# Performance work log

Hardware: AMD Instinct MI355X
Metric: run time of the kernel (lower is better)

Reference implementation:

```python
import jax, jax.numpy as jnp
import numpy as np
import math

B, S, E, H = 2, 2048, 1024, 16
Dh = E // H

def setup_inputs() -> dict:
    key = jax.random.key(0)
    ks = jax.random.split(key, 11)
    s_in = 1.0 / math.sqrt(E)
    return {
        "key": jax.random.normal(ks[0], (B, S, E), jnp.float32),
        "query": jax.random.normal(ks[1], (B, S, E), jnp.float32),
        "value": jax.random.normal(ks[2], (B, S, E), jnp.float32),
        "Wq": jax.random.normal(ks[3], (E, E), jnp.float32) * s_in,
        "bq": jnp.zeros((E,), jnp.float32),
        "Wk": jax.random.normal(ks[4], (E, E), jnp.float32) * s_in,
        "bk": jnp.zeros((E,), jnp.float32),
        "Wv": jax.random.normal(ks[5], (E, E), jnp.float32) * s_in,
        "bv": jnp.zeros((E,), jnp.float32),
        "Wo": jax.random.normal(ks[6], (E, E), jnp.float32) * s_in,
        "bo": jnp.zeros((E,), jnp.float32),
    }

def _split_heads(x):
    # [B,S,E] -> [B,H,S,Dh]
    b, s, _ = x.shape
    return x.reshape(b, s, H, Dh).transpose(0, 2, 1, 3)

def reference(key, query, value, Wq, bq, Wk, bk, Wv, bv, Wo, bo):
    k = _split_heads(key @ Wk.T + bk)
    q = _split_heads(query @ Wq.T + bq)
    v = _split_heads(value @ Wv.T + bv)
    scale = 1.0 / math.sqrt(Dh)
    # [B,H,S,S] score matrix (faithful to naive implementation)
    scores = jnp.einsum("bhqd,bhkd->bhqk", q, k) * scale
    probs = jax.nn.softmax(scores, axis=-1)
    attn = jnp.einsum("bhqk,bhkd->bhqd", probs, v)  # [B,H,S,Dh]
    out = attn.transpose(0, 2, 1, 3).reshape(key.shape[0], key.shape[1], E)
    return out @ Wo.T + bo
```

## Files before the change

### kernel.cpp

```cpp
#include <hip/hip_runtime.h>
#include <hip/hip_bf16.h>
#include <stdint.h>

typedef short    bf16x8 __attribute__((ext_vector_type(8)));
typedef float    f32x4  __attribute__((ext_vector_type(4)));
typedef float    f32x16 __attribute__((ext_vector_type(16)));
typedef uint32_t u32x2  __attribute__((ext_vector_type(2)));
typedef uint32_t u32x4  __attribute__((ext_vector_type(4)));
typedef uint16_t u16x4  __attribute__((ext_vector_type(4)));

#define DEV __device__ __forceinline__
#define AS1 __attribute__((address_space(1)))
#define AS3 __attribute__((address_space(3)))

#define SM_SCALE 0.18033688011112042f

DEV uint32_t pk_bf16(float lo, float hi) {
    uint32_t r;
    asm("v_cvt_pk_bf16_f32 %0, %1, %2" : "=v"(r) : "v"(lo), "v"(hi));
    return r;
}

DEV void gload_lds16(const uint16_t* g, uint16_t* l) {
    __builtin_amdgcn_global_load_lds((AS1 const uint32_t*)g, (AS3 uint32_t*)l, 16, 0, 0);
}

DEV void plane32_swap(uint32_t& a, uint32_t& b) {
    asm("v_permlane32_swap_b32 %0, %1" : "+v"(a), "+v"(b));
}

__global__ __launch_bounds__(256) void cast_all(
    const float* __restrict__ w0, const float* __restrict__ w1,
    const float* __restrict__ w2, const float* __restrict__ w3,
    const float* __restrict__ aq, const float* __restrict__ ak, const float* __restrict__ av,
    uint16_t* __restrict__ ws)
{
    const int y = blockIdx.y;
    const float* s;
    uint16_t* d;
    if (y < 4) {
        if (blockIdx.x >= 512) return;
        s = (y == 0) ? w0 : (y == 1) ? w1 : (y == 2) ? w2 : w3;
        d = ws + ((size_t)y << 20);
    } else {
        s = (y == 4) ? aq : (y == 5) ? ak : av;
        d = ws + (size_t)(1 << 22) + ((size_t)(y - 4) << 22);
    }
    const float m = (y == 0) ? SM_SCALE : 1.0f;
    const size_t i = ((size_t)blockIdx.x * 256 + threadIdx.x) * 8;
    float4 a = *reinterpret_cast<const float4*>(s + i);
    float4 b = *reinterpret_cast<const float4*>(s + i + 4);
    u32x4 w;
    w[0] = pk_bf16(a.x * m, a.y * m); w[1] = pk_bf16(a.z * m, a.w * m);
    w[2] = pk_bf16(b.x * m, b.y * m); w[3] = pk_bf16(b.z * m, b.w * m);
    *reinterpret_cast<u32x4*>(d + i) = w;
}

__global__ __launch_bounds__(256) void gemm_qkv(
    const uint16_t* __restrict__ Qc, const uint16_t* __restrict__ Kc, const uint16_t* __restrict__ Vc,
    const uint16_t* __restrict__ wqc, const uint16_t* __restrict__ wkc, const uint16_t* __restrict__ wvc,
    const float* __restrict__ bq, const float* __restrict__ bk, const float* __restrict__ bv,
    uint16_t* __restrict__ Qb, uint16_t* __restrict__ Kb, uint16_t* __restrict__ Vt)
{
    constexpr int Kd = 1024, N = 1024;
    __shared__ uint16_t Al[2][128 * 32];
    __shared__ uint16_t Bl[2][128 * 32];

    const int z = blockIdx.z;
    const uint16_t* A = (z == 0) ? Qc : (z == 1) ? Kc : Vc;
    const uint16_t* W = (z == 0) ? wqc : (z == 1) ? wkc : wvc;
    const float* bias = (z == 0) ? bq : (z == 1) ? bk : bv;
    const float bs = (z == 0) ? SM_SCALE : 1.0f;

    const int brow = blockIdx.x * 128;
    const int bcol = blockIdx.y * 128;
    const int t = threadIdx.x, lane = t & 63, wid = t >> 6;
    const int wr = wid >> 1, wc = wid & 1;

    const int srow = wid * 16 + (lane >> 2);
    const int scol = (lane & 3) * 8;
    const uint16_t* aA = A + (size_t)(brow + srow) * Kd + scol;
    const uint16_t* aW = W + (size_t)(bcol + srow) * Kd + scol;
    uint16_t* lA = &Al[0][srow * 32 + scol];
    uint16_t* lB = &Bl[0][srow * 32 + scol];

    f32x4 acc[4][4];
#pragma unroll
    for (int i = 0; i < 4; ++i)
#pragma unroll
        for (int j = 0; j < 4; ++j)
#pragma unroll
            for (int e = 0; e < 4; ++e) acc[i][j][e] = 0.f;

    const int frow = lane & 15;
    const int koff = (lane >> 4) * 8;

    for (int k0 = 0; k0 < Kd; k0 += 64) {
#pragma unroll
        for (int p = 0; p < 2; ++p) {
            gload_lds16(aA + k0 + p * 32, lA + p * 4096);
            gload_lds16(aA + k0 + p * 32 + (size_t)64 * Kd, lA + p * 4096 + 2048);
            gload_lds16(aW + k0 + p * 32, lB + p * 4096);
            gload_lds16(aW + k0 + p * 32 + (size_t)64 * Kd, lB + p * 4096 + 2048);
        }
        __syncthreads();

#pragma unroll
        for (int p = 0; p < 2; ++p) {
            bf16x8 af[4], bfr[4];
#pragma unroll
            for (int fr = 0; fr < 4; ++fr)
                af[fr] = *reinterpret_cast<const bf16x8*>(&Al[p][(wr * 64 + fr * 16 + frow) * 32 + koff]);
#pragma unroll
            for (int fc = 0; fc < 4; ++fc)
                bfr[fc] = *reinterpret_cast<const bf16x8*>(&Bl[p][(wc * 64 + fc * 16 + frow) * 32 + koff]);
#pragma unroll
            for (int fr = 0; fr < 4; ++fr)
#pragma unroll
                for (int fc = 0; fc < 4; ++fc)
                    acc[fr][fc] = __builtin_amdgcn_mfma_f32_16x16x32_bf16(af[fr], bfr[fc], acc[fr][fc], 0, 0, 0);
        }
        __syncthreads();
    }

    const int m0 = brow + wr * 64;
    const int n0 = bcol + wc * 64;
    if (z < 2) {
        uint16_t* Cb = (z == 0) ? Qb : Kb;
#pragma unroll
        for (int fc = 0; fc < 4; ++fc) {
            const int col = n0 + fc * 16 + frow;
            const float bia = bias[col] * bs;
#pragma unroll
            for (int fr = 0; fr < 4; ++fr) {
                const int mrow = m0 + fr * 16 + (lane >> 4) * 4;
                f32x4 a = acc[fr][fc];
                uint32_t w01 = pk_bf16(a[0] + bia, a[1] + bia);
                uint32_t w23 = pk_bf16(a[2] + bia, a[3] + bia);
                Cb[(size_t)(mrow + 0) * N + col] = (uint16_t)(w01 & 0xffff);
                Cb[(size_t)(mrow + 1) * N + col] = (uint16_t)(w01 >> 16);
                Cb[(size_t)(mrow + 2) * N + col] = (uint16_t)(w23 & 0xffff);
                Cb[(size_t)(mrow + 3) * N + col] = (uint16_t)(w23 >> 16);
            }
        }
    } else {
#pragma unroll
        for (int fc = 0; fc < 4; ++fc) {
            const int col = n0 + fc * 16 + frow;
            const int hh = col >> 6, dd = col & 63;
            const float bia = bias[col];
#pragma unroll
            for (int fr = 0; fr < 4; ++fr) {
                const int mrow = m0 + fr * 16 + (lane >> 4) * 4;
                const int bb = mrow >> 11, ss = mrow & 2047;
                f32x4 a = acc[fr][fc];
                uint32_t w01 = pk_bf16(a[0] + bia, a[1] + bia);
                uint32_t w23 = pk_bf16(a[2] + bia, a[3] + bia);
                u16x4 pv;
                pv[0] = (uint16_t)(w01 & 0xffff); pv[1] = (uint16_t)(w01 >> 16);
                pv[2] = (uint16_t)(w23 & 0xffff); pv[3] = (uint16_t)(w23 >> 16);
                *reinterpret_cast<u16x4*>(&Vt[(size_t)((bb * 16 + hh) * 64 + dd) * 2048 + ss]) = pv;
            }
        }
    }
}

__global__ __launch_bounds__(256, 4) void attn_kernel(
    const uint16_t* __restrict__ Qb, const uint16_t* __restrict__ Kb,
    const uint16_t* __restrict__ Vt, uint16_t* __restrict__ At)
{
    constexpr int S = 2048, E = 1024;
    __shared__ uint16_t Kl[2][64 * 72];
    __shared__ uint16_t Vl[2][64 * 72];

    const int bh = blockIdx.y;
    const int b = bh >> 4, h = bh & 15;
    const int t = threadIdx.x;
    const int lane = t & 63, wid = t >> 6;
    const int lo = lane & 31, hi = lane >> 5;
    const int half = wid >> 1;
    const int q0 = blockIdx.x * 64 + (wid & 1) * 32;

    bf16x8 qf[4];
    {
        const uint16_t* qrow = Qb + (size_t)(b * S + q0 + lo) * E + h * 64;
#pragma unroll
        for (int kk = 0; kk < 4; ++kk)
            qf[kk] = *reinterpret_cast<const bf16x8*>(qrow + kk * 16 + hi * 8);
    }

    f32x16 oacc[2];
#pragma unroll
    for (int i = 0; i < 16; ++i) { oacc[0][i] = 0.f; oacc[1][i] = 0.f; }
    float mrun = -1e30f, lsum = 0.f;

    const uint16_t* Kbase = Kb + (size_t)(b * S) * E + h * 64;
    const uint16_t* Vbase = Vt + (size_t)(bh * 64) * S;

    const int r = t >> 2, seg = t & 3;
    const int lds_off = r * 72 + seg * 16;

#pragma unroll 1
    for (int i = 0; i < 16; ++i) {
        {
            const uint16_t* ksa = Kbase + (size_t)(i * 64 + r) * E + seg * 16;
            const uint16_t* vsa = Vbase + (size_t)r * S + i * 64 + seg * 16;
            const uint16_t* ksb = ksa + (size_t)1024 * E;
            const uint16_t* vsb = vsa + 1024;
            u32x4 k0a = *reinterpret_cast<const u32x4*>(ksa);
            u32x4 k1a = *reinterpret_cast<const u32x4*>(ksa + 8);
            u32x4 v0a = *reinterpret_cast<const u32x4*>(vsa);
            u32x4 v1a = *reinterpret_cast<const u32x4*>(vsa + 8);
            u32x4 k0b = *reinterpret_cast<const u32x4*>(ksb);
            u32x4 k1b = *reinterpret_cast<const u32x4*>(ksb + 8);
            u32x4 v0b = *reinterpret_cast<const u32x4*>(vsb);
            u32x4 v1b = *reinterpret_cast<const u32x4*>(vsb + 8);
            *reinterpret_cast<u32x4*>(&Kl[0][lds_off])     = k0a;
            *reinterpret_cast<u32x4*>(&Kl[0][lds_off + 8]) = k1a;
            *reinterpret_cast<u32x4*>(&Vl[0][lds_off])     = v0a;
            *reinterpret_cast<u32x4*>(&Vl[0][lds_off + 8]) = v1a;
            *reinterpret_cast<u32x4*>(&Kl[1][lds_off])     = k0b;
            *reinterpret_cast<u32x4*>(&Kl[1][lds_off + 8]) = k1b;
            *reinterpret_cast<u32x4*>(&Vl[1][lds_off])     = v0b;
            *reinterpret_cast<u32x4*>(&Vl[1][lds_off + 8]) = v1b;
        }
        __syncthreads();

        f32x16 sacc[2];
#pragma unroll
        for (int j = 0; j < 16; ++j) { sacc[0][j] = 0.f; sacc[1][j] = 0.f; }
        __builtin_amdgcn_s_setprio(1);
#pragma unroll
        for (int kk = 0; kk < 4; ++kk) {
            bf16x8 ka0 = *reinterpret_cast<const bf16x8*>(&Kl[half][lo * 72 + kk * 16 + hi * 8]);
            bf16x8 ka1 = *reinterpret_cast<const bf16x8*>(&Kl[half][(32 + lo) * 72 + kk * 16 + hi * 8]);
            sacc[0] = __builtin_amdgcn_mfma_f32_32x32x16_bf16(ka0, qf[kk], sacc[0], 0, 0, 0);
            sacc[1] = __builtin_amdgcn_mfma_f32_32x32x16_bf16(ka1, qf[kk], sacc[1], 0, 0, 0);
        }
        __builtin_amdgcn_s_setprio(0);

        float tm[16];
#pragma unroll
        for (int j = 0; j < 16; ++j) tm[j] = fmaxf(sacc[0][j], sacc[1][j]);
#pragma unroll
        for (int s = 8; s > 0; s >>= 1)
#pragma unroll
            for (int j = 0; j < 8; ++j)
                if (j < s) tm[j] = fmaxf(tm[j], tm[j + s]);
        float pmax = tm[0];
        pmax = fmaxf(pmax, __shfl_xor(pmax, 32, 64));

        if (!__all(pmax - mrun <= 3.0f)) {
            float mnew = fmaxf(mrun, pmax);
            float corr = __builtin_amdgcn_exp2f(mrun - mnew);
            lsum *= corr;
#pragma unroll
            for (int j = 0; j < 16; ++j) { oacc[0][j] *= corr; oacc[1][j] *= corr; }
            mrun = mnew;
        }

        uint32_t w[16];
        float ps0 = 0.f, ps1 = 0.f, ps2 = 0.f, ps3 = 0.f;
#pragma unroll
        for (int kf = 0; kf < 2; ++kf)
#pragma unroll
            for (int j = 0; j < 8; ++j) {
                float pa = __builtin_amdgcn_exp2f(sacc[kf][2 * j]     - mrun);
                float pb = __builtin_amdgcn_exp2f(sacc[kf][2 * j + 1] - mrun);
                if (j & 1) { ps0 += pa; ps1 += pb; } else { ps2 += pa; ps3 += pb; }
                w[kf * 8 + j] = pk_bf16(pa, pb);
            }
        lsum += (ps0 + ps1) + (ps2 + ps3);

        __builtin_amdgcn_s_setprio(1);
#pragma unroll
        for (int ks = 0; ks < 4; ++ks) {
            const int base = (ks >> 1) * 8 + (ks & 1) * 4;
            uint32_t p0 = w[base + 0], p2 = w[base + 2];
            uint32_t p1 = w[base + 1], p3 = w[base + 3];
            plane32_swap(p0, p2);
            plane32_swap(p1, p3);
            u32x4 pw; pw[0] = p0; pw[1] = p1; pw[2] = p2; pw[3] = p3;
            bf16x8 pf = __builtin_bit_cast(bf16x8, pw);
#pragma unroll
            for (int df = 0; df < 2; ++df) {
                bf16x8 vf = *reinterpret_cast<const bf16x8*>(&Vl[half][(df * 32 + lo) * 72 + ks * 16 + hi * 8]);
                oacc[df] = __builtin_amdgcn_mfma_f32_32x32x16_bf16(vf, pf, oacc[df], 0, 0, 0);
            }
        }
        __builtin_amdgcn_s_setprio(0);
        __syncthreads();
    }

    lsum += __shfl_xor(lsum, 32, 64);

    float* ob  = reinterpret_cast<float*>(&Kl[0][0]);
    float* mlb = reinterpret_cast<float*>(&Vl[0][0]);
    const int w2 = wid & 1;
    if (half == 1) {
        float* dst = ob + (w2 * 64 + lane) * 36;
#pragma unroll
        for (int df = 0; df < 2; ++df)
#pragma unroll
            for (int j = 0; j < 16; ++j) dst[df * 16 + j] = oacc[df][j];
        mlb[(w2 * 64 + lane) * 2]     = mrun;
        mlb[(w2 * 64 + lane) * 2 + 1] = lsum;
    }
    __syncthreads();
    if (half == 0) {
        const float* src = ob + (w2 * 64 + lane) * 36;
        const float m1 = mlb[(w2 * 64 + lane) * 2];
        const float l1 = mlb[(w2 * 64 + lane) * 2 + 1];
        const float m  = fmaxf(mrun, m1);
        const float c0 = __builtin_amdgcn_exp2f(mrun - m);
        const float c1 = __builtin_amdgcn_exp2f(m1 - m);
        const float inv = 1.0f / (c0 * lsum + c1 * l1);
        uint16_t* orow = At + (size_t)(b * S + q0 + lo) * E + h * 64;
#pragma unroll
        for (int df = 0; df < 2; ++df)
#pragma unroll
            for (int g = 0; g < 4; ++g) {
                float e0 = (c0 * oacc[df][4 * g + 0] + c1 * src[df * 16 + 4 * g + 0]) * inv;
                float e1 = (c0 * oacc[df][4 * g + 1] + c1 * src[df * 16 + 4 * g + 1]) * inv;
                float e2 = (c0 * oacc[df][4 * g + 2] + c1 * src[df * 16 + 4 * g + 2]) * inv;
                float e3 = (c0 * oacc[df][4 * g + 3] + c1 * src[df * 16 + 4 * g + 3]) * inv;
                uint32_t w01 = pk_bf16(e0, e1);
                uint32_t w23 = pk_bf16(e2, e3);
                u32x2 o2; o2[0] = w01; o2[1] = w23;
                *reinterpret_cast<u32x2*>(orow + df * 32 + 8 * g + 4 * hi) = o2;
            }
    }
}

__global__ __launch_bounds__(256) void gemm_out(
    const uint16_t* __restrict__ Atn, const uint16_t* __restrict__ woc,
    const float* __restrict__ bo, float* __restrict__ out)
{
    constexpr int Kd = 1024, N = 1024;
    __shared__ uint16_t Al[2][128 * 32];
    __shared__ uint16_t Bl[2][128 * 32];

    const int brow = blockIdx.x * 128;
    const int bcol = blockIdx.y * 128;
    const int t = threadIdx.x, lane = t & 63, wid = t >> 6;
    const int wr = wid >> 1, wc = wid & 1;

    const int srow = wid * 16 + (lane >> 2);
    const int scol = (lane & 3) * 8;
    const uint16_t* aA = Atn + (size_t)(brow + srow) * Kd + scol;
    const uint16_t* aW = woc + (size_t)(bcol + srow) * Kd + scol;
    uint16_t* lA = &Al[0][srow * 32 + scol];
    uint16_t* lB = &Bl[0][srow * 32 + scol];

    f32x4 acc[4][4];
#pragma unroll
    for (int i = 0; i < 4; ++i)
#pragma unroll
        for (int j = 0; j < 4; ++j)
#pragma unroll
            for (int e = 0; e < 4; ++e) acc[i][j][e] = 0.f;

    const int frow = lane & 15;
    const int koff = (lane >> 4) * 8;

    for (int k0 = 0; k0 < Kd; k0 += 64) {
#pragma unroll
        for (int p = 0; p < 2; ++p) {
            gload_lds16(aA + k0 + p * 32, lA + p * 4096);
            gload_lds16(aA + k0 + p * 32 + (size_t)64 * Kd, lA + p * 4096 + 2048);
            gload_lds16(aW + k0 + p * 32, lB + p * 4096);
            gload_lds16(aW + k0 + p * 32 + (size_t)64 * Kd, lB + p * 4096 + 2048);
        }
        __syncthreads();

#pragma unroll
        for (int p = 0; p < 2; ++p) {
            bf16x8 af[4], bfr[4];
#pragma unroll
            for (int fr = 0; fr < 4; ++fr)
                af[fr] = *reinterpret_cast<const bf16x8*>(&Al[p][(wr * 64 + fr * 16 + frow) * 32 + koff]);
#pragma unroll
            for (int fc = 0; fc < 4; ++fc)
                bfr[fc] = *reinterpret_cast<const bf16x8*>(&Bl[p][(wc * 64 + fc * 16 + frow) * 32 + koff]);
#pragma unroll
            for (int fr = 0; fr < 4; ++fr)
#pragma unroll
                for (int fc = 0; fc < 4; ++fc)
                    acc[fr][fc] = __builtin_amdgcn_mfma_f32_16x16x32_bf16(af[fr], bfr[fc], acc[fr][fc], 0, 0, 0);
        }
        __syncthreads();
    }

    const int m0 = brow + wr * 64;
    const int n0 = bcol + wc * 64;
#pragma unroll
    for (int fc = 0; fc < 4; ++fc) {
        const int col = n0 + fc * 16 + frow;
        const float bia = bo[col];
#pragma unroll
        for (int fr = 0; fr < 4; ++fr) {
            const int mrow = m0 + fr * 16 + (lane >> 4) * 4;
#pragma unroll
            for (int j = 0; j < 4; ++j)
                out[(size_t)(mrow + j) * N + col] = acc[fr][fc][j] + bia;
        }
    }
}

extern "C" void kernel_launch(void* const* d_in, const int* in_sizes, int n_in,
                              void* d_out, int out_size, void* d_ws, size_t ws_size,
                              hipStream_t stream)
{
    const float* key   = (const float*)d_in[0];
    const float* query = (const float*)d_in[1];
    const float* value = (const float*)d_in[2];
    const float* Wq = (const float*)d_in[3];
    const float* bq = (const float*)d_in[4];
    const float* Wk = (const float*)d_in[5];
    const float* bk = (const float*)d_in[6];
    const float* Wv = (const float*)d_in[7];
    const float* bv = (const float*)d_in[8];
    const float* Wo = (const float*)d_in[9];
    const float* bo = (const float*)d_in[10];

    uint16_t* ws = (uint16_t*)d_ws;
    uint16_t* wqc = ws;
    uint16_t* wkc = ws + ((size_t)1 << 20);
    uint16_t* wvc = ws + ((size_t)2 << 20);
    uint16_t* woc = ws + ((size_t)3 << 20);
    uint16_t* Qc  = ws + ((size_t)1 << 22);
    uint16_t* Kc  = ws + ((size_t)2 << 22);
    uint16_t* Vc  = ws + ((size_t)3 << 22);
    uint16_t* Qb  = ws + ((size_t)4 << 22);
    uint16_t* Kb  = ws + ((size_t)5 << 22);
    uint16_t* Vt  = ws + ((size_t)6 << 22);
    uint16_t* At  = Qc;
    float* out = (float*)d_out;

    cast_all<<<dim3(2048, 7), 256, 0, stream>>>(Wq, Wk, Wv, Wo, query, key, value, ws);
    gemm_qkv<<<dim3(32, 8, 3), 256, 0, stream>>>(Qc, Kc, Vc, wqc, wkc, wvc,
                                                 bq, bk, bv, Qb, Kb, Vt);
    attn_kernel<<<dim3(32, 32), 256, 0, stream>>>(Qb, Kb, Vt, At);
    gemm_out<<<dim3(32, 8), 256, 0, stream>>>(At, woc, bo, out);
}
```

Before: 135.0 us.

## Load K/V MFMA fragments directly from global memory and swizzle attention block order

The attention kernel drops its LDS staging of K and V tiles and the per-iteration __syncthreads barriers. Each wave now reads its MFMA operand fragments straight from global memory, relying on L2 and MALL for reuse across the blocks of the same head. The grid is flattened to 1D with a swizzle that spreads consecutive blocks across 8 groups, likely so blocks sharing a head land on the same XCD's L2. In exchange, each wave issues more global loads whose latency is no longer hidden by staging, and reuse within a block is lost.

```diff
diff --git a/kernel.cpp b/kernel.cpp
--- a/kernel.cpp
+++ b/kernel.cpp
@@ -170,16 +170,18 @@
     const uint16_t* __restrict__ Vt, uint16_t* __restrict__ At)
 {
     constexpr int S = 2048, E = 1024;
-    __shared__ uint16_t Kl[2][64 * 72];
-    __shared__ uint16_t Vl[2][64 * 72];
-
-    const int bh = blockIdx.y;
+    __shared__ float ob[128 * 36];
+    __shared__ float mlb[128 * 2];
+
+    const int bid = blockIdx.x;
+    const int swz = (bid & 7) * 128 + (bid >> 3);
+    const int bh = swz >> 5;
     const int b = bh >> 4, h = bh & 15;
     const int t = threadIdx.x;
     const int lane = t & 63, wid = t >> 6;
     const int lo = lane & 31, hi = lane >> 5;
     const int half = wid >> 1;
-    const int q0 = blockIdx.x * 64 + (wid & 1) * 32;
+    const int q0 = (swz & 31) * 64 + (wid & 1) * 32;
 
     bf16x8 qf[4];
     {
@@ -194,37 +196,15 @@
     for (int i = 0; i < 16; ++i) { oacc[0][i] = 0.f; oacc[1][i] = 0.f; }
     float mrun = -1e30f, lsum = 0.f;
 
-    const uint16_t* Kbase = Kb + (size_t)(b * S) * E + h * 64;
-    const uint16_t* Vbase = Vt + (size_t)(bh * 64) * S;
-
-    const int r = t >> 2, seg = t & 3;
-    const int lds_off = r * 72 + seg * 16;
+    const uint16_t* k0p = Kb + (size_t)(b * S + half * 1024 + lo) * E + h * 64 + hi * 8;
+    const uint16_t* k1p = k0p + (size_t)32 * E;
+    const uint16_t* v0p = Vt + (size_t)(bh * 64 + lo) * S + half * 1024 + hi * 8;
+    const uint16_t* v1p = v0p + (size_t)32 * S;
 
 #pragma unroll 1
     for (int i = 0; i < 16; ++i) {
-        {
-            const uint16_t* ksa = Kbase + (size_t)(i * 64 + r) * E + seg * 16;
-            const uint16_t* vsa = Vbase + (size_t)r * S + i * 64 + seg * 16;
-            const uint16_t* ksb = ksa + (size_t)1024 * E;
-            const uint16_t* vsb = vsa + 1024;
-            u32x4 k0a = *reinterpret_cast<const u32x4*>(ksa);
-            u32x4 k1a = *reinterpret_cast<const u32x4*>(ksa + 8);
-            u32x4 v0a = *reinterpret_cast<const u32x4*>(vsa);
-            u32x4 v1a = *reinterpret_cast<const u32x4*>(vsa + 8);
-            u32x4 k0b = *reinterpret_cast<const u32x4*>(ksb);
-            u32x4 k1b = *reinterpret_cast<const u32x4*>(ksb + 8);
-            u32x4 v0b = *reinterpret_cast<const u32x4*>(vsb);
-            u32x4 v1b = *reinterpret_cast<const u32x4*>(vsb + 8);
-            *reinterpret_cast<u32x4*>(&Kl[0][lds_off])     = k0a;
-            *reinterpret_cast<u32x4*>(&Kl[0][lds_off + 8]) = k1a;
-            *reinterpret_cast<u32x4*>(&Vl[0][lds_off])     = v0a;
-            *reinterpret_cast<u32x4*>(&Vl[0][lds_off + 8]) = v1a;
-            *reinterpret_cast<u32x4*>(&Kl[1][lds_off])     = k0b;
-            *reinterpret_cast<u32x4*>(&Kl[1][lds_off + 8]) = k1b;
-            *reinterpret_cast<u32x4*>(&Vl[1][lds_off])     = v0b;
-            *reinterpret_cast<u32x4*>(&Vl[1][lds_off + 8]) = v1b;
-        }
-        __syncthreads();
+        const size_t ko = (size_t)i * 64 * E;
+        const int    vo = i * 64;
 
         f32x16 sacc[2];
 #pragma unroll
@@ -232,8 +212,8 @@
         __builtin_amdgcn_s_setprio(1);
 #pragma unroll
         for (int kk = 0; kk < 4; ++kk) {
-            bf16x8 ka0 = *reinterpret_cast<const bf16x8*>(&Kl[half][lo * 72 + kk * 16 + hi * 8]);
-            bf16x8 ka1 = *reinterpret_cast<const bf16x8*>(&Kl[half][(32 + lo) * 72 + kk * 16 + hi * 8]);
+            bf16x8 ka0 = *reinterpret_cast<const bf16x8*>(k0p + ko + kk * 16);
+            bf16x8 ka1 = *reinterpret_cast<const bf16x8*>(k1p + ko + kk * 16);
             sacc[0] = __builtin_amdgcn_mfma_f32_32x32x16_bf16(ka0, qf[kk], sacc[0], 0, 0, 0);
             sacc[1] = __builtin_amdgcn_mfma_f32_32x32x16_bf16(ka1, qf[kk], sacc[1], 0, 0, 0);
         }
@@ -282,20 +262,16 @@
             plane32_swap(p1, p3);
             u32x4 pw; pw[0] = p0; pw[1] = p1; pw[2] = p2; pw[3] = p3;
             bf16x8 pf = __builtin_bit_cast(bf16x8, pw);
-#pragma unroll
-            for (int df = 0; df < 2; ++df) {
-                bf16x8 vf = *reinterpret_cast<const bf16x8*>(&Vl[half][(df * 32 + lo) * 72 + ks * 16 + hi * 8]);
-                oacc[df] = __builtin_amdgcn_mfma_f32_32x32x16_bf16(vf, pf, oacc[df], 0, 0, 0);
-            }
+            bf16x8 vf0 = *reinterpret_cast<const bf16x8*>(v0p + vo + ks * 16);
+            bf16x8 vf1 = *reinterpret_cast<const bf16x8*>(v1p + vo + ks * 16);
+            oacc[0] = __builtin_amdgcn_mfma_f32_32x32x16_bf16(vf0, pf, oacc[0], 0, 0, 0);
+            oacc[1] = __builtin_amdgcn_mfma_f32_32x32x16_bf16(vf1, pf, oacc[1], 0, 0, 0);
         }
         __builtin_amdgcn_s_setprio(0);
-        __syncthreads();
     }
 
     lsum += __shfl_xor(lsum, 32, 64);
 
-    float* ob  = reinterpret_cast<float*>(&Kl[0][0]);
-    float* mlb = reinterpret_cast<float*>(&Vl[0][0]);
     const int w2 = wid & 1;
     if (half == 1) {
         float* dst = ob + (w2 * 64 + lane) * 36;
@@ -440,6 +416,6 @@
     cast_all<<<dim3(2048, 7), 256, 0, stream>>>(Wq, Wk, Wv, Wo, query, key, value, ws);
     gemm_qkv<<<dim3(32, 8, 3), 256, 0, stream>>>(Qc, Kc, Vc, wqc, wkc, wvc,
                                                  bq, bk, bv, Qb, Kb, Vt);
-    attn_kernel<<<dim3(32, 32), 256, 0, stream>>>(Qb, Kb, Vt, At);
+    attn_kernel<<<dim3(1024), 256, 0, stream>>>(Qb, Kb, Vt, At);
     gemm_out<<<dim3(32, 8), 256, 0, stream>>>(At, woc, bo, out);
 }
```

New measurement: 201.7 us. 1.49x slower.

## Fuse fp32-to-bf16 activation cast into QKV projection GEMM

Applied to the files above, without the earlier changes.

Removes the separate cast pass over query/key/value. The QKV GEMM now loads fp32 activations directly into LDS and converts them to bf16 while building MFMA fragments. This avoids writing and re-reading bf16 copies of the activations, at the cost of doubled A-tile global/LDS bytes and extra conversion work inside the GEMM inner loop. The workspace layout is compacted accordingly.

```diff
diff --git a/kernel.cpp b/kernel.cpp
--- a/kernel.cpp
+++ b/kernel.cpp
@@ -21,7 +21,7 @@
     return r;
 }
 
-DEV void gload_lds16(const uint16_t* g, uint16_t* l) {
+DEV void gload_lds16(const void* g, void* l) {
     __builtin_amdgcn_global_load_lds((AS1 const uint32_t*)g, (AS3 uint32_t*)l, 16, 0, 0);
 }
 
@@ -29,23 +29,14 @@
     asm("v_permlane32_swap_b32 %0, %1" : "+v"(a), "+v"(b));
 }
 
-__global__ __launch_bounds__(256) void cast_all(
+__global__ __launch_bounds__(256) void cast_w(
     const float* __restrict__ w0, const float* __restrict__ w1,
     const float* __restrict__ w2, const float* __restrict__ w3,
-    const float* __restrict__ aq, const float* __restrict__ ak, const float* __restrict__ av,
     uint16_t* __restrict__ ws)
 {
     const int y = blockIdx.y;
-    const float* s;
-    uint16_t* d;
-    if (y < 4) {
-        if (blockIdx.x >= 512) return;
-        s = (y == 0) ? w0 : (y == 1) ? w1 : (y == 2) ? w2 : w3;
-        d = ws + ((size_t)y << 20);
-    } else {
-        s = (y == 4) ? aq : (y == 5) ? ak : av;
-        d = ws + (size_t)(1 << 22) + ((size_t)(y - 4) << 22);
-    }
+    const float* s = (y == 0) ? w0 : (y == 1) ? w1 : (y == 2) ? w2 : w3;
+    uint16_t* d = ws + ((size_t)y << 20);
     const float m = (y == 0) ? SM_SCALE : 1.0f;
     const size_t i = ((size_t)blockIdx.x * 256 + threadIdx.x) * 8;
     float4 a = *reinterpret_cast<const float4*>(s + i);
@@ -57,17 +48,17 @@
 }
 
 __global__ __launch_bounds__(256) void gemm_qkv(
-    const uint16_t* __restrict__ Qc, const uint16_t* __restrict__ Kc, const uint16_t* __restrict__ Vc,
+    const float* __restrict__ Aq, const float* __restrict__ Ak, const float* __restrict__ Av,
     const uint16_t* __restrict__ wqc, const uint16_t* __restrict__ wkc, const uint16_t* __restrict__ wvc,
     const float* __restrict__ bq, const float* __restrict__ bk, const float* __restrict__ bv,
     uint16_t* __restrict__ Qb, uint16_t* __restrict__ Kb, uint16_t* __restrict__ Vt)
 {
     constexpr int Kd = 1024, N = 1024;
-    __shared__ uint16_t Al[2][128 * 32];
+    __shared__ float    Afl[4][128 * 16];
     __shared__ uint16_t Bl[2][128 * 32];
 
     const int z = blockIdx.z;
-    const uint16_t* A = (z == 0) ? Qc : (z == 1) ? Kc : Vc;
+    const float*    A = (z == 0) ? Aq : (z == 1) ? Ak : Av;
     const uint16_t* W = (z == 0) ? wqc : (z == 1) ? wkc : wvc;
     const float* bias = (z == 0) ? bq : (z == 1) ? bk : bv;
     const float bs = (z == 0) ? SM_SCALE : 1.0f;
@@ -78,11 +69,10 @@
     const int wr = wid >> 1, wc = wid & 1;
 
     const int srow = wid * 16 + (lane >> 2);
-    const int scol = (lane & 3) * 8;
-    const uint16_t* aA = A + (size_t)(brow + srow) * Kd + scol;
-    const uint16_t* aW = W + (size_t)(bcol + srow) * Kd + scol;
-    uint16_t* lA = &Al[0][srow * 32 + scol];
-    uint16_t* lB = &Bl[0][srow * 32 + scol];
+    const float* aA = A + (size_t)(brow + srow) * Kd + (lane & 3) * 4;
+    float* lAf = &Afl[0][0] + (size_t)wid * 256 + (size_t)(lane >> 2) * 16 + (lane & 3) * 4;
+    const uint16_t* aW = W + (size_t)(bcol + srow) * Kd + (lane & 3) * 8;
+    uint16_t* lB = &Bl[0][srow * 32 + (lane & 3) * 8];
 
     f32x4 acc[4][4];
 #pragma unroll
@@ -93,13 +83,20 @@
             for (int e = 0; e < 4; ++e) acc[i][j][e] = 0.f;
 
     const int frow = lane & 15;
+    const int qsel = (lane >> 5);
+    const int foff = ((lane >> 4) & 1) * 8;
     const int koff = (lane >> 4) * 8;
 
     for (int k0 = 0; k0 < Kd; k0 += 64) {
 #pragma unroll
+        for (int q = 0; q < 4; ++q) {
+#pragma unroll
+            for (int rh = 0; rh < 2; ++rh)
+                gload_lds16(aA + k0 + q * 16 + (size_t)rh * 64 * Kd,
+                            lAf + q * 2048 + rh * 1024);
+        }
+#pragma unroll
         for (int p = 0; p < 2; ++p) {
-            gload_lds16(aA + k0 + p * 32, lA + p * 4096);
-            gload_lds16(aA + k0 + p * 32 + (size_t)64 * Kd, lA + p * 4096 + 2048);
             gload_lds16(aW + k0 + p * 32, lB + p * 4096);
             gload_lds16(aW + k0 + p * 32 + (size_t)64 * Kd, lB + p * 4096 + 2048);
         }
@@ -109,8 +106,15 @@
         for (int p = 0; p < 2; ++p) {
             bf16x8 af[4], bfr[4];
 #pragma unroll
-            for (int fr = 0; fr < 4; ++fr)
-                af[fr] = *reinterpret_cast<const bf16x8*>(&Al[p][(wr * 64 + fr * 16 + frow) * 32 + koff]);
+            for (int fr = 0; fr < 4; ++fr) {
+                const float* ap = &Afl[2 * p + qsel][(wr * 64 + fr * 16 + frow) * 16 + foff];
+                f32x4 lo4 = *reinterpret_cast<const f32x4*>(ap);
+                f32x4 hi4 = *reinterpret_cast<const f32x4*>(ap + 4);
+                u32x4 aw;
+                aw[0] = pk_bf16(lo4[0], lo4[1]); aw[1] = pk_bf16(lo4[2], lo4[3]);
+                aw[2] = pk_bf16(hi4[0], hi4[1]); aw[3] = pk_bf16(hi4[2], hi4[3]);
+                af[fr] = __builtin_bit_cast(bf16x8, aw);
+            }
 #pragma unroll
             for (int fc = 0; fc < 4; ++fc)
                 bfr[fc] = *reinterpret_cast<const bf16x8*>(&Bl[p][(wc * 64 + fc * 16 + frow) * 32 + koff]);
@@ -428,17 +432,14 @@
     uint16_t* wkc = ws + ((size_t)1 << 20);
     uint16_t* wvc = ws + ((size_t)2 << 20);
     uint16_t* woc = ws + ((size_t)3 << 20);
-    uint16_t* Qc  = ws + ((size_t)1 << 22);
-    uint16_t* Kc  = ws + ((size_t)2 << 22);
-    uint16_t* Vc  = ws + ((size_t)3 << 22);
-    uint16_t* Qb  = ws + ((size_t)4 << 22);
-    uint16_t* Kb  = ws + ((size_t)5 << 22);
-    uint16_t* Vt  = ws + ((size_t)6 << 22);
-    uint16_t* At  = Qc;
+    uint16_t* Qb  = ws + ((size_t)1 << 22);
+    uint16_t* Kb  = ws + ((size_t)2 << 22);
+    uint16_t* Vt  = ws + ((size_t)3 << 22);
+    uint16_t* At  = ws + ((size_t)4 << 22);
     float* out = (float*)d_out;
 
-    cast_all<<<dim3(2048, 7), 256, 0, stream>>>(Wq, Wk, Wv, Wo, query, key, value, ws);
-    gemm_qkv<<<dim3(32, 8, 3), 256, 0, stream>>>(Qc, Kc, Vc, wqc, wkc, wvc,
+    cast_w<<<dim3(512, 4), 256, 0, stream>>>(Wq, Wk, Wv, Wo, ws);
+    gemm_qkv<<<dim3(32, 8, 3), 256, 0, stream>>>(query, key, value, wqc, wkc, wvc,
                                                  bq, bk, bv, Qb, Kb, Vt);
     attn_kernel<<<dim3(32, 32), 256, 0, stream>>>(Qb, Kb, Vt, At);
     gemm_out<<<dim3(32, 8), 256, 0, stream>>>(At, woc, bo, out);
```

Result: slower. 141.7 us (+5.0%).
